# Optimization experiments

Measured on AMD Instinct MI355X. Metric: run time of the kernel, lower is better.

The kernel has to match this reference:

```python
import jax, jax.numpy as jnp
import numpy as np

B, S, E, H, MAXLEN = 2, 2048, 1024, 16, 2048


def _level_indices(seq_len: int, base: int = 2) -> np.ndarray:
    """Vectorized version of get_level_index_weak over the full (target, source) grid.
    indices[t, s] = min(level, 2) for s < t, else 0. Runs in O(log S) passes."""
    tt = np.broadcast_to(np.arange(seq_len)[:, None], (seq_len, seq_len)).astype(np.int64).copy()
    ss = np.broadcast_to(np.arange(seq_len)[None, :], (seq_len, seq_len)).astype(np.int64).copy()
    res = np.zeros((seq_len, seq_len), np.int64)
    done = ~(ss < tt)  # only source < target positions get a level; rest stay 0
    while not done.all():
        l = np.floor(np.log2(np.maximum(tt, 1).astype(np.float64))).astype(np.int64)
        v = (np.int64(1) << l)
        hit = (~done) & (ss < v)
        res[hit] = l[hit] + 1
        done |= hit
        step = ~done
        tt[step] -= v[step]
        ss[step] -= v[step]
    return np.minimum(res, 2).astype(np.int32)


def setup_inputs() -> dict:
    key = jax.random.key(0)
    ks = jax.random.split(key, 10)
    sc = 0.02
    return {
        "x": jax.random.normal(ks[0], (B, S, E), dtype=jnp.float32),
        "attention_mask": jax.random.randint(ks[1], (B, S), 0, 2, dtype=jnp.int32),
        "level_indices": jnp.asarray(_level_indices(S, 2)),
        "Wq": jax.random.normal(ks[2], (E, E), dtype=jnp.float32) * sc,
        "bq": jnp.zeros((E,), jnp.float32),
        "Wk": jax.random.normal(ks[3], (E, E), dtype=jnp.float32) * sc,
        "bk": jnp.zeros((E,), jnp.float32),
        "Wv": jax.random.normal(ks[4], (E, E), dtype=jnp.float32) * sc,
        "bv": jnp.zeros((E,), jnp.float32),
        "hier": jax.random.normal(ks[5], (MAXLEN, H, 3), dtype=jnp.float32),
        "Wo": jax.random.normal(ks[6], (E, E), dtype=jnp.float32) * sc,
        "bo": jnp.zeros((E,), jnp.float32),
    }


def reference(x, attention_mask, level_indices, Wq, bq, Wk, bk, Wv, bv, hier, Wo, bo):
    b, s, e = x.shape
    h = hier.shape[1]
    dh = e // h
    # q/k are computed by the original module but never used; kept for fidelity (zero grads).
    q = x @ Wq.T + bq
    k = x @ Wk.T + bk
    v = (x @ Wv.T + bv).reshape(b, s, h, dh).transpose(0, 2, 1, 3)  # [B,H,S,Dh]
    lev = level_indices[:s, :s]  # [S,S] int, values in {0,1,2}
    # Faithful torch.gather semantics: weights[b,h,i,j] = hier[b, h, lev[i,j]]
    w3 = hier[:b]                      # [B,H,3]
    weights = w3[:, :, lev]            # [B,H,S,S]
    decay = jnp.power(jnp.float32(0.5), lev.astype(x.dtype))  # [S,S]
    weights = weights * decay
    weights = weights / (jnp.sum(weights, axis=-1, keepdims=True) + 1e-8)
    weights = jnp.where(attention_mask[:, None, None, :] == 0, jnp.float32(0.0), weights)
    out = jnp.einsum('bhij,bhjd->bhid', weights, v)  # [B,H,S,Dh]
    out = out.transpose(0, 2, 1, 3).reshape(b, s, e)
    return out @ Wo.T + bo
```

## Files before the change

### kernel.cpp

```cpp
#include <hip/hip_runtime.h>
#include <cstdint>
#include <cstddef>

constexpr int Sn = 2048;
constexpr int En = 1024;
constexpr int Bn = 2;
constexpr int Hn = 16;
constexpr int CHUNK = 32;
constexpr int NCH = Sn / CHUNK;
constexpr int Mtot = Bn * Sn;
constexpr int GCH = Mtot / CHUNK;

typedef __bf16 bf16x8 __attribute__((ext_vector_type(8)));
typedef float  f32x4  __attribute__((ext_vector_type(4)));

__device__ __forceinline__ unsigned short f2bf(float f) {
    union { float f; uint32_t u; } v; v.f = f;
    const uint32_t u = v.u;
    return (unsigned short)((u + 0x7fffu + ((u >> 16) & 1u)) >> 16);
}
__device__ __forceinline__ float bf2f(unsigned short s) {
    union { uint32_t u; float f; } v; v.u = (uint32_t)s << 16; return v.f;
}

constexpr int XN = Bn * Sn * En;
constexpr int WN = En * En;

__global__ __launch_bounds__(256)
void cast2(const float* __restrict__ x, const float* __restrict__ Wv,
           unsigned short* __restrict__ xb, unsigned short* __restrict__ Wvb)
{
    const int i = (blockIdx.x * 256 + threadIdx.x) * 4;
    const float* src; unsigned short* dst; int off;
    if (i < XN) { src = x;  dst = xb;  off = i; }
    else        { src = Wv; dst = Wvb; off = i - XN; }
    const float4 v = *(const float4*)(src + off);
    ushort4 o;
    o.x = f2bf(v.x); o.y = f2bf(v.y); o.z = f2bf(v.z); o.w = f2bf(v.w);
    *(ushort4*)(dst + off) = o;
}

#define LOAD4(k0, r0, r1, r2, r3)                    \
    r0 = *(const uint4*)(gA0 + (k0));                \
    r1 = *(const uint4*)(gA0 + (k0) + 32);           \
    r2 = *(const uint4*)(gB0 + (k0));                \
    r3 = *(const uint4*)(gB0 + (k0) + 32);

#define STORE4(r0, r1, r2, r3)                       \
    *lA0 = r0; *lA1 = r1;                            \
    *lB0 = r2; *lB1 = r3;

#define COMPUTE()                                                                              \
    {                                                                                          \
        bf16x8 af[4][2], bfr[2][2];                                                            \
        _Pragma("unroll")                                                                      \
        for (int i = 0; i < 4; ++i)                                                            \
            _Pragma("unroll")                                                                  \
            for (int kh = 0; kh < 2; ++kh)                                                     \
                af[i][kh] = *(const bf16x8*)&As[((wr * 4 + i) * 2 + kh) * 512 + lane * 8];      \
        _Pragma("unroll")                                                                      \
        for (int j = 0; j < 2; ++j)                                                            \
            _Pragma("unroll")                                                                  \
            for (int kh = 0; kh < 2; ++kh)                                                     \
                bfr[j][kh] = *(const bf16x8*)&Bs[((wc * 2 + j) * 2 + kh) * 512 + lane * 8];     \
        _Pragma("unroll")                                                                      \
        for (int kh = 0; kh < 2; ++kh)                                                         \
            _Pragma("unroll")                                                                  \
            for (int i = 0; i < 4; ++i)                                                        \
                _Pragma("unroll")                                                              \
                for (int j = 0; j < 2; ++j)                                                    \
                    acc[i][j] = __builtin_amdgcn_mfma_f32_16x16x32_bf16(af[i][kh], bfr[j][kh], \
                                                                        acc[i][j], 0, 0, 0);   \
    }

template<bool APPLY_MASK, bool OUT_BF16, bool FUSE_CSUM>
__global__ __launch_bounds__(512, 2)
void gemm128(const unsigned short* __restrict__ A, const unsigned short* __restrict__ Bw,
             const float* __restrict__ bias, const int* __restrict__ mask,
             void* __restrict__ Cv, float* __restrict__ csum)
{
    __shared__ __align__(16) unsigned short As[128 * 64];
    __shared__ __align__(16) unsigned short Bs[128 * 64];

    const int tid  = threadIdx.x;
    const int lane = tid & 63;
    const int wv   = tid >> 6;
    const int wr   = wv >> 2;
    const int wc   = wv & 3;
    const int id   = blockIdx.y * 8 + blockIdx.x;
    const int xcd  = id & 7;
    const int slot = id >> 3;
    const int by   = xcd * 4 + (slot >> 3);
    const int bx   = slot & 7;
    const int bm   = by * 128;
    const int bn   = bx * 128;
    const int m16  = lane & 15;
    const int kq   = lane >> 4;

    f32x4 acc[4][2] = {};

    const unsigned short* gA0 = A  + (size_t)(bm + 16 * wv + m16) * En + kq * 8;
    const unsigned short* gB0 = Bw + (size_t)(bn + 16 * wv + m16) * En + kq * 8;
    uint4* lA0 = (uint4*)&As[(wv * 2 + 0) * 512 + lane * 8];
    uint4* lA1 = (uint4*)&As[(wv * 2 + 1) * 512 + lane * 8];
    uint4* lB0 = (uint4*)&Bs[(wv * 2 + 0) * 512 + lane * 8];
    uint4* lB1 = (uint4*)&Bs[(wv * 2 + 1) * 512 + lane * 8];

    uint4 p0, p1, p2, p3;
    uint4 q0, q1, q2, q3;

    LOAD4(0, p0, p1, p2, p3);
#pragma unroll 1
    for (int it = 0; it < 8; ++it) {
        const int kbase = it * 128;
        __syncthreads();
        STORE4(p0, p1, p2, p3);
        __syncthreads();
        LOAD4(kbase + 64, q0, q1, q2, q3);
        COMPUTE();

        __syncthreads();
        STORE4(q0, q1, q2, q3);
        __syncthreads();
        if (it < 7) { LOAD4(kbase + 128, p0, p1, p2, p3); }
        COMPUTE();
    }

    float colsum[2][2] = {{0.0f, 0.0f}, {0.0f, 0.0f}};
#pragma unroll
    for (int i = 0; i < 4; ++i) {
        const int r0_ = bm + wr * 64 + i * 16 + kq * 4;
#pragma unroll
        for (int j = 0; j < 2; ++j) {
            const int c0 = bn + wc * 32 + j * 16 + m16;
            const float bcol = bias[c0];
#pragma unroll
            for (int r = 0; r < 4; ++r) {
                const int row = r0_ + r;
                float val = acc[i][j][r] + bcol;
                if (APPLY_MASK) val = (mask[row] == 0) ? 0.0f : val;
                if (FUSE_CSUM) colsum[i >> 1][j] += val;
                if (OUT_BF16)
                    ((unsigned short*)Cv)[(size_t)row * En + c0] = f2bf(val);
                else
                    ((float*)Cv)[(size_t)row * En + c0] = val;
            }
        }
    }

    if (FUSE_CSUM) {
        const int gc0 = 4 * by + 2 * wr;
#pragma unroll
        for (int g = 0; g < 2; ++g)
#pragma unroll
            for (int j = 0; j < 2; ++j) {
                float s = colsum[g][j];
                s += __shfl_xor(s, 16, 64);
                s += __shfl_xor(s, 32, 64);
                if (kq == 0)
                    csum[(size_t)(gc0 + g) * En + bn + wc * 32 + j * 16 + m16] = s;
            }
    }
}

__global__ __launch_bounds__(256)
void combine(const unsigned short* __restrict__ vm, const float* __restrict__ csum,
             const float* __restrict__ hier, const float* __restrict__ Wo,
             unsigned short* __restrict__ Wob, unsigned short* __restrict__ opre)
{
    __shared__ __align__(16) unsigned short tile[CHUNK * 256];

    const int tid = threadIdx.x;
    const int ec0 = blockIdx.x * 256;
    const int c   = blockIdx.y;
    const int b   = blockIdx.z;

    {
        const int lane16 = tid & 31;
        const int rbase  = tid >> 5;
        const size_t g0 = ((size_t)b * Sn + c * CHUNK) * En + ec0 + lane16 * 8;
#pragma unroll
        for (int r4 = 0; r4 < 4; ++r4) {
            const int row = r4 * 8 + rbase;
            *(uint4*)&tile[row * 256 + lane16 * 8] =
                *(const uint4*)(vm + g0 + (size_t)row * En);
        }
    }

    {
        const int fid = (blockIdx.z * 64 + blockIdx.y) * 4 + blockIdx.x;
        const int base = fid * 2048 + tid * 4;
#pragma unroll
        for (int half = 0; half < 2; ++half) {
            const int off = base + half * 1024;
            const float4 v = *(const float4*)(Wo + off);
            ushort4 o;
            o.x = f2bf(v.x); o.y = f2bf(v.y); o.z = f2bf(v.z); o.w = f2bf(v.w);
            *(ushort4*)(Wob + off) = o;
        }
    }

    const int e = ec0 + tid;
    const int h = e >> 6;
    const float w0 = hier[((size_t)b * Hn + h) * 3 + 0];
    const float w1 = hier[((size_t)b * Hn + h) * 3 + 1] * 0.5f;
    const float w2 = hier[((size_t)b * Hn + h) * 3 + 2] * 0.25f;

    float run = 0.0f, T = 0.0f;
    {
        const float* cp = csum + (size_t)b * NCH * En + e;
#pragma unroll 16
        for (int c2 = 0; c2 < NCH; ++c2) {
            const float v = cp[(size_t)c2 * En];
            T += v;
            run += (c2 < c) ? v : 0.0f;
        }
    }

    __syncthreads();

    float prev = 0.0f;
    const size_t base = ((size_t)b * Sn + c * CHUNK) * En + e;

#pragma unroll
    for (int t = 0; t < CHUNK; ++t) {
        const int i = c * CHUNK + t;
        const float cur = bf2f(tile[t * 256 + tid]);
        float num, Z;
        if (i & 1) {
            num = w2 * (run - prev) + w1 * prev + w0 * (T - run);
            Z = (float)(i - 1) * w2 + w1 + (float)(Sn - i) * w0 + 1e-8f;
        } else {
            num = w2 * run + w0 * (T - run);
            Z = (float)i * w2 + (float)(Sn - i) * w0 + 1e-8f;
        }
        opre[base + (size_t)t * En] = f2bf(num / Z);
        run += cur;
        prev = cur;
    }
}

extern "C" void kernel_launch(void* const* d_in, const int* in_sizes, int n_in,
                              void* d_out, int out_size, void* d_ws, size_t ws_size,
                              hipStream_t stream)
{
    const float* x    = (const float*)d_in[0];
    const int*   mask = (const int*)d_in[1];
    const float* Wv   = (const float*)d_in[7];
    const float* bv   = (const float*)d_in[8];
    const float* hier = (const float*)d_in[9];
    const float* Wo   = (const float*)d_in[10];
    const float* bo   = (const float*)d_in[11];
    float* out = (float*)d_out;

    char* ws = (char*)d_ws;
    unsigned short* xb    = (unsigned short*)ws;  ws += (size_t)Mtot * En * 2;
    unsigned short* Wvb   = (unsigned short*)ws;  ws += (size_t)En * En * 2;
    unsigned short* Wob   = (unsigned short*)ws;  ws += (size_t)En * En * 2;
    unsigned short* vmb   = (unsigned short*)ws;  ws += (size_t)Mtot * En * 2;
    float*          csum  = (float*)ws;           ws += (size_t)GCH * En * 4;
    unsigned short* opreb = (unsigned short*)ws;  ws += (size_t)Mtot * En * 2;

    cast2<<<dim3((XN + WN) / 1024), dim3(256), 0, stream>>>(x, Wv, xb, Wvb);

    dim3 gemm_grid(8, 32);
    dim3 gemm_threads(512);

    gemm128<true, true, true><<<gemm_grid, gemm_threads, 0, stream>>>(xb, Wvb, bv, mask, vmb, csum);
    combine<<<dim3(En / 256, NCH, Bn), dim3(256), 0, stream>>>(vmb, csum, hier, Wo, Wob, opreb);
    gemm128<false, false, false><<<gemm_grid, gemm_threads, 0, stream>>>(opreb, Wob, bo, nullptr, out, nullptr);
}
```

Measured before the change: 164.0 us.

## Fuse V-projection, combine, and output GEMM into one cooperative kernel

Replaces the three launches (V GEMM, combine, output GEMM) with a single cooperative kernel that uses grid-wide syncs between phases. The per-chunk prefix scan over column sums, which each combine block used to redo from scratch, is now computed once by four blocks into prefix and total buffers. The aim is to cut kernel launch gaps and the redundant prefix work. In exchange it adds three grid barriers plus a serial scan phase in which most blocks sit idle, and it relies on all 256 blocks being co-resident.

```diff
diff --git a/kernel.cpp b/kernel.cpp
--- a/kernel.cpp
+++ b/kernel.cpp
@@ -1,6 +1,9 @@
 #include <hip/hip_runtime.h>
+#include <hip/hip_cooperative_groups.h>
 #include <cstdint>
 #include <cstddef>
+
+namespace cg = cooperative_groups;
 
 constexpr int Sn = 2048;
 constexpr int En = 1024;
@@ -74,20 +77,17 @@
     }
 
 template<bool APPLY_MASK, bool OUT_BF16, bool FUSE_CSUM>
-__global__ __launch_bounds__(512, 2)
-void gemm128(const unsigned short* __restrict__ A, const unsigned short* __restrict__ Bw,
-             const float* __restrict__ bias, const int* __restrict__ mask,
-             void* __restrict__ Cv, float* __restrict__ csum)
+__device__ __forceinline__
+void gemm_body(unsigned short* As, unsigned short* Bs,
+               const unsigned short* __restrict__ A, const unsigned short* __restrict__ Bw,
+               const float* __restrict__ bias, const int* __restrict__ mask,
+               void* __restrict__ Cv, float* __restrict__ csum,
+               int id, int tid)
 {
-    __shared__ __align__(16) unsigned short As[128 * 64];
-    __shared__ __align__(16) unsigned short Bs[128 * 64];
-
-    const int tid  = threadIdx.x;
     const int lane = tid & 63;
     const int wv   = tid >> 6;
     const int wr   = wv >> 2;
     const int wc   = wv & 3;
-    const int id   = blockIdx.y * 8 + blockIdx.x;
     const int xcd  = id & 7;
     const int slot = id >> 3;
     const int by   = xcd * 4 + (slot >> 3);
@@ -163,81 +163,114 @@
     }
 }
 
-__global__ __launch_bounds__(256)
-void combine(const unsigned short* __restrict__ vm, const float* __restrict__ csum,
-             const float* __restrict__ hier, const float* __restrict__ Wo,
-             unsigned short* __restrict__ Wob, unsigned short* __restrict__ opre)
+__global__ __launch_bounds__(512, 2)
+void fused(const unsigned short* __restrict__ xb, const unsigned short* __restrict__ Wvb,
+           const float* __restrict__ bv, const int* __restrict__ mask,
+           unsigned short* __restrict__ vmb, float* __restrict__ csum,
+           float* __restrict__ prefexc, float* __restrict__ Tbuf,
+           const float* __restrict__ hier, const float* __restrict__ Wo,
+           unsigned short* __restrict__ Wob, unsigned short* __restrict__ opreb,
+           const float* __restrict__ bo, float* __restrict__ out)
 {
-    __shared__ __align__(16) unsigned short tile[CHUNK * 256];
+    __shared__ __align__(16) unsigned short As[128 * 64];
+    __shared__ __align__(16) unsigned short Bs[128 * 64];
 
     const int tid = threadIdx.x;
-    const int ec0 = blockIdx.x * 256;
-    const int c   = blockIdx.y;
-    const int b   = blockIdx.z;
-
-    {
-        const int lane16 = tid & 31;
-        const int rbase  = tid >> 5;
-        const size_t g0 = ((size_t)b * Sn + c * CHUNK) * En + ec0 + lane16 * 8;
-#pragma unroll
-        for (int r4 = 0; r4 < 4; ++r4) {
-            const int row = r4 * 8 + rbase;
-            *(uint4*)&tile[row * 256 + lane16 * 8] =
-                *(const uint4*)(vm + g0 + (size_t)row * En);
-        }
-    }
-
-    {
-        const int fid = (blockIdx.z * 64 + blockIdx.y) * 4 + blockIdx.x;
-        const int base = fid * 2048 + tid * 4;
-#pragma unroll
-        for (int half = 0; half < 2; ++half) {
-            const int off = base + half * 1024;
-            const float4 v = *(const float4*)(Wo + off);
-            ushort4 o;
-            o.x = f2bf(v.x); o.y = f2bf(v.y); o.z = f2bf(v.z); o.w = f2bf(v.w);
-            *(ushort4*)(Wob + off) = o;
-        }
-    }
-
-    const int e = ec0 + tid;
-    const int h = e >> 6;
-    const float w0 = hier[((size_t)b * Hn + h) * 3 + 0];
-    const float w1 = hier[((size_t)b * Hn + h) * 3 + 1] * 0.5f;
-    const float w2 = hier[((size_t)b * Hn + h) * 3 + 2] * 0.25f;
-
-    float run = 0.0f, T = 0.0f;
-    {
+    const int rb  = blockIdx.y * 8 + blockIdx.x;
+
+    gemm_body<true, true, true>(As, Bs, xb, Wvb, bv, mask, vmb, csum, rb, tid);
+
+    __threadfence();
+    cg::this_grid().sync();
+
+    if (rb < 4) {
+        const int t = rb * 512 + tid;
+        const int b = t >> 10, e = t & 1023;
         const float* cp = csum + (size_t)b * NCH * En + e;
-#pragma unroll 16
+        float* pp = prefexc + (size_t)b * NCH * En + e;
+        float run = 0.0f;
+#pragma unroll 8
         for (int c2 = 0; c2 < NCH; ++c2) {
             const float v = cp[(size_t)c2 * En];
-            T += v;
-            run += (c2 < c) ? v : 0.0f;
-        }
-    }
-
-    __syncthreads();
-
-    float prev = 0.0f;
-    const size_t base = ((size_t)b * Sn + c * CHUNK) * En + e;
-
-#pragma unroll
-    for (int t = 0; t < CHUNK; ++t) {
-        const int i = c * CHUNK + t;
-        const float cur = bf2f(tile[t * 256 + tid]);
-        float num, Z;
-        if (i & 1) {
-            num = w2 * (run - prev) + w1 * prev + w0 * (T - run);
-            Z = (float)(i - 1) * w2 + w1 + (float)(Sn - i) * w0 + 1e-8f;
-        } else {
-            num = w2 * run + w0 * (T - run);
-            Z = (float)i * w2 + (float)(Sn - i) * w0 + 1e-8f;
-        }
-        opre[base + (size_t)t * En] = f2bf(num / Z);
-        run += cur;
-        prev = cur;
-    }
+            pp[(size_t)c2 * En] = run;
+            run += v;
+        }
+        Tbuf[b * En + e] = run;
+    }
+
+    __threadfence();
+    cg::this_grid().sync();
+
+    {
+        const int half = tid >> 8;
+        const int t8   = tid & 255;
+        const int vb   = rb * 2 + half;
+        const int bx   = vb & 3;
+        const int cc   = (vb >> 2) & 63;
+        const int b    = vb >> 8;
+        const int ec0  = bx * 256;
+        unsigned short* tile = half ? Bs : As;
+
+        {
+            const int lane16 = t8 & 31;
+            const int rbase  = t8 >> 5;
+            const size_t g0 = ((size_t)b * Sn + cc * CHUNK) * En + ec0 + lane16 * 8;
+#pragma unroll
+            for (int r4 = 0; r4 < 4; ++r4) {
+                const int row = r4 * 8 + rbase;
+                *(uint4*)&tile[row * 256 + lane16 * 8] =
+                    *(const uint4*)(vmb + g0 + (size_t)row * En);
+            }
+        }
+
+        {
+            const int base = vb * 2048 + t8 * 4;
+#pragma unroll
+            for (int hf = 0; hf < 2; ++hf) {
+                const int off = base + hf * 1024;
+                const float4 v = *(const float4*)(Wo + off);
+                ushort4 o;
+                o.x = f2bf(v.x); o.y = f2bf(v.y); o.z = f2bf(v.z); o.w = f2bf(v.w);
+                *(ushort4*)(Wob + off) = o;
+            }
+        }
+
+        const int e = ec0 + t8;
+        const int h = e >> 6;
+        const float w0 = hier[((size_t)b * Hn + h) * 3 + 0];
+        const float w1 = hier[((size_t)b * Hn + h) * 3 + 1] * 0.5f;
+        const float w2 = hier[((size_t)b * Hn + h) * 3 + 2] * 0.25f;
+
+        float run = prefexc[(size_t)(b * NCH + cc) * En + e];
+        const float T = Tbuf[b * En + e];
+
+        __syncthreads();
+
+        float prev = 0.0f;
+        const size_t base = ((size_t)b * Sn + cc * CHUNK) * En + e;
+
+#pragma unroll
+        for (int t = 0; t < CHUNK; ++t) {
+            const int i = cc * CHUNK + t;
+            const float cur = bf2f(tile[t * 256 + t8]);
+            float num, Z;
+            if (i & 1) {
+                num = w2 * (run - prev) + w1 * prev + w0 * (T - run);
+                Z = (float)(i - 1) * w2 + w1 + (float)(Sn - i) * w0 + 1e-8f;
+            } else {
+                num = w2 * run + w0 * (T - run);
+                Z = (float)i * w2 + (float)(Sn - i) * w0 + 1e-8f;
+            }
+            opreb[base + (size_t)t * En] = f2bf(num / Z);
+            run += cur;
+            prev = cur;
+        }
+    }
+
+    __threadfence();
+    cg::this_grid().sync();
+
+    gemm_body<false, false, false>(As, Bs, opreb, Wob, bo, nullptr, out, nullptr, rb, tid);
 }
 
 extern "C" void kernel_launch(void* const* d_in, const int* in_sizes, int n_in,
@@ -260,13 +293,17 @@
     unsigned short* vmb   = (unsigned short*)ws;  ws += (size_t)Mtot * En * 2;
     float*          csum  = (float*)ws;           ws += (size_t)GCH * En * 4;
     unsigned short* opreb = (unsigned short*)ws;  ws += (size_t)Mtot * En * 2;
+    float*          pref  = (float*)ws;           ws += (size_t)GCH * En * 4;
+    float*          Tbuf  = (float*)ws;           ws += (size_t)Bn * En * 4;
 
     cast2<<<dim3((XN + WN) / 1024), dim3(256), 0, stream>>>(x, Wv, xb, Wvb);
 
-    dim3 gemm_grid(8, 32);
-    dim3 gemm_threads(512);
-
-    gemm128<true, true, true><<<gemm_grid, gemm_threads, 0, stream>>>(xb, Wvb, bv, mask, vmb, csum);
-    combine<<<dim3(En / 256, NCH, Bn), dim3(256), 0, stream>>>(vmb, csum, hier, Wo, Wob, opreb);
-    gemm128<false, false, false><<<gemm_grid, gemm_threads, 0, stream>>>(opreb, Wob, bo, nullptr, out, nullptr);
-}
+    void* args[] = {
+        (void*)&xb, (void*)&Wvb, (void*)&bv, (void*)&mask,
+        (void*)&vmb, (void*)&csum, (void*)&pref, (void*)&Tbuf,
+        (void*)&hier, (void*)&Wo, (void*)&Wob, (void*)&opreb,
+        (void*)&bo, (void*)&out
+    };
+    hipLaunchCooperativeKernel((const void*)fused, dim3(8, 32), dim3(512),
+                               args, 0, stream);
+}
```

Result: slower. 391.4 us (+138.7%).
